# Optimization experiments

Measured on AMD Instinct MI355X. Metric: run time of the kernel, lower is better.

Reference implementation:

```python
import jax, jax.numpy as jnp
import numpy as np

HIDDEN = 1024
HEADS = 16
HEAD = HIDDEN // HEADS  # 64, rotary_emb_dim == head dim
B = 8
S = 1024  # max_seqlen; all sequences full length
WINDOW = (64, 64)  # sliding_window=128 -> (64, 64)
ROPE_BASE = 10000.0


def _rope_cos_sin(seqlen, dim, base):
    inv_freq = 1.0 / (base ** (jnp.arange(0, dim, 2, dtype=jnp.float32) / dim))
    t = jnp.arange(seqlen, dtype=jnp.float32)
    freqs = jnp.outer(t, inv_freq)  # [S, dim/2]
    return jnp.cos(freqs), jnp.sin(freqs)


def _apply_rope(x, cos, sin):
    # x: [B, S, H, D], non-interleaved rotary over full head dim
    d2 = cos.shape[-1]
    x1, x2 = x[..., :d2], x[..., d2:]
    c = cos[None, :, None, :]
    s = sin[None, :, None, :]
    return jnp.concatenate([x1 * c - x2 * s, x2 * c + x1 * s], axis=-1)


def setup_inputs() -> dict:
    key = jax.random.key(0)
    k1, k2, k3 = jax.random.split(key, 3)
    hidden_states = jax.random.normal(k1, (B * S, HIDDEN), dtype=jnp.float32)
    cu_seqlens = jnp.arange(B + 1, dtype=jnp.int32) * S
    indices = jnp.arange(B * S, dtype=jnp.int32)
    attn_mask = jnp.ones((B, S), dtype=jnp.int32)
    Wqkv = jax.random.normal(k2, (3 * HIDDEN, HIDDEN), dtype=jnp.float32) * 0.02
    Wo = jax.random.normal(k3, (HIDDEN, HIDDEN), dtype=jnp.float32) * 0.02
    return {
        'hidden_states': hidden_states,
        'cu_seqlens': cu_seqlens,
        'max_seqlen': S,
        'indices': indices,
        'attn_mask': attn_mask,
        'Wqkv': Wqkv,
        'Wo': Wo,
    }


def reference(hidden_states, cu_seqlens, max_seqlen, indices, attn_mask, Wqkv, Wo):
    # QKV projection on unpadded tokens: [T, 3*H*D]
    qkv = hidden_states @ Wqkv.T
    qkv = qkv.reshape(B, S, 3, HEADS, HEAD)
    # Rotary positions reset per sequence; all sequences are full length S.
    cos, sin = _rope_cos_sin(S, HEAD, ROPE_BASE)
    q = _apply_rope(qkv[:, :, 0], cos, sin)
    k = _apply_rope(qkv[:, :, 1], cos, sin)
    v = qkv[:, :, 2]
    scores = jnp.einsum('bshd,bthd->bhst', q, k) / jnp.sqrt(jnp.float32(HEAD))
    # sliding-window mask: key j visible to query i iff i-left <= j <= i+right
    i = jnp.arange(S)[:, None]
    j = jnp.arange(S)[None, :]
    win = (j >= i - WINDOW[0]) & (j <= i + WINDOW[1])  # [S, S]
    key_mask = attn_mask.astype(bool)[:, None, None, :]  # [B,1,1,S]
    mask = win[None, None, :, :] & key_mask
    scores = jnp.where(mask, scores, jnp.finfo(scores.dtype).min)
    probs = jax.nn.softmax(scores, axis=-1)
    attn = jnp.einsum('bhst,bthd->bshd', probs, v).reshape(B * S, HIDDEN)
    return attn @ Wo.T
```

## Files before the change

### kernel.cpp

```cpp
#include <hip/hip_runtime.h>


typedef __attribute__((ext_vector_type(8))) short short8;
typedef __attribute__((ext_vector_type(4))) float f32x4;

#define SEQ   1024
#define NHEAD 16
#define HEADD 64
#define NTOK  8192

__device__ __forceinline__ unsigned short f2bf(float x) {
  unsigned u = __float_as_uint(x);
  u += 0x7fffu + ((u >> 16) & 1u);
  return (unsigned short)(u >> 16);
}

__device__ __forceinline__ void gload_lds16(const void* g, void* l) {
  __builtin_amdgcn_global_load_lds((__attribute__((address_space(1))) void*)(g),
                                   (__attribute__((address_space(3))) void*)(l),
                                   16, 0, 0);
}

__global__ __launch_bounds__(256) void prep(
    const float* __restrict__ hidden, const float* __restrict__ Wqkv,
    const float* __restrict__ Wo,
    unsigned short* __restrict__ hb, unsigned short* __restrict__ wqb,
    unsigned short* __restrict__ wob, float2* __restrict__ tab) {
  int bid = blockIdx.x;
  const float* in; unsigned short* out; int i;
  if (bid < 8192)       { in = hidden; out = hb;  i = bid * 256 + threadIdx.x; }
  else if (bid < 11264) { in = Wqkv;   out = wqb; i = (bid - 8192) * 256 + threadIdx.x; }
  else if (bid < 12288) { in = Wo;     out = wob; i = (bid - 11264) * 256 + threadIdx.x; }
  else {
    int j = (bid - 12288) * 256 + threadIdx.x;
    int s = j >> 5, d = j & 31;
    float inv = exp2f(-(float)d * 0.41524101186092034f);
    float sn, cs;
    sincosf((float)s * inv, &sn, &cs);
    tab[j] = make_float2(cs, sn);
    return;
  }
  float4 v = ((const float4*)in)[i];
  ushort4 o;
  o.x = f2bf(v.x); o.y = f2bf(v.y); o.z = f2bf(v.z); o.w = f2bf(v.w);
  ((ushort4*)out)[i] = o;
}

__global__ __launch_bounds__(256) void gemm_qkv_rope(
    const unsigned short* __restrict__ A,
    const unsigned short* __restrict__ W,
    const float2* __restrict__ tab,
    unsigned short* __restrict__ qb,
    unsigned short* __restrict__ kb,
    unsigned short* __restrict__ vt)
{
  __shared__ unsigned short As[128 * 32];
  __shared__ unsigned short Bs[128 * 32];
  const int tid  = threadIdx.x;
  const int wave = tid >> 6, lane = tid & 63;
  const int quad = lane >> 4, l15 = lane & 15;
  const int bid  = blockIdx.x;
  const int xcd  = bid & 7, idx = bid >> 3;
  const int rb   = xcd * 8 + (idx & 7);
  const int cb   = idx >> 3;
  const int row0 = rb * 128;
  const int col0 = cb * 128;
  const int mrow = (wave >> 1) * 64;
  const int ncol = (wave & 1) * 64;
  const int qs8  = (quad ^ ((l15 >> 1) & 3)) * 8;

  f32x4 acc[4][4];
#pragma unroll
  for (int i = 0; i < 4; i++)
#pragma unroll
    for (int j = 0; j < 4; j++) acc[i][j] = (f32x4){0.f, 0.f, 0.f, 0.f};

  for (int k0 = 0; k0 < 1024; k0 += 32) {
#pragma unroll
    for (int i = 0; i < 2; i++) {
      int p = i * 256 + tid;
      int r = p >> 2, c = p & 3;
      int cs = c ^ ((r >> 1) & 3);
      gload_lds16(A + (size_t)(row0 + r) * 1024 + k0 + cs * 8, &As[p * 8]);
      gload_lds16(W + (size_t)(col0 + r) * 1024 + k0 + cs * 8, &Bs[p * 8]);
    }
    __syncthreads();
    short8 af[4], bf[4];
#pragma unroll
    for (int mt = 0; mt < 4; mt++)
      af[mt] = *(const short8*)&As[(mrow + mt * 16 + l15) * 32 + qs8];
#pragma unroll
    for (int nt = 0; nt < 4; nt++)
      bf[nt] = *(const short8*)&Bs[(ncol + nt * 16 + l15) * 32 + qs8];
#pragma unroll
    for (int mt = 0; mt < 4; mt++)
#pragma unroll
      for (int nt = 0; nt < 4; nt++)
        acc[mt][nt] = __builtin_amdgcn_mfma_f32_16x16x32_bf16(af[mt], bf[nt],
                                                              acc[mt][nt], 0, 0, 0);
    __syncthreads();
  }

  const int colw  = col0 + ncol;
  const int which = colw >> 10;
  const int h     = (colw >> 6) & 15;
  const int rowg  = row0 + mrow;

  if (which == 2) {
#pragma unroll
    for (int mt = 0; mt < 4; mt++) {
      int rbase = rowg + mt * 16 + quad * 4;
      int b = rbase >> 10, s = rbase & 1023;
#pragma unroll
      for (int c = 0; c < 4; c++) {
        int d = c * 16 + l15;
        ushort4 o;
        o.x = f2bf(acc[mt][c][0]); o.y = f2bf(acc[mt][c][1]);
        o.z = f2bf(acc[mt][c][2]); o.w = f2bf(acc[mt][c][3]);
        *(ushort4*)&vt[((size_t)((b * 16 + h) * 64 + d)) * 1024 + s] = o;
      }
    }
  } else {
    unsigned short* dst = (which == 0) ? qb : kb;
    const float scale = (which == 0) ? 0.125f : 1.0f;
#pragma unroll
    for (int mt = 0; mt < 4; mt++) {
#pragma unroll
      for (int r = 0; r < 4; r++) {
        int row = rowg + mt * 16 + quad * 4 + r;
        int b = row >> 10, s = row & 1023;
        size_t base = (size_t)((b * 16 + h) * 1024 + s) * 64;
        float2 t0 = tab[s * 32 + l15];
        float2 t1 = tab[s * 32 + 16 + l15];
        float x1a = acc[mt][0][r], x2a = acc[mt][2][r];
        float x1b = acc[mt][1][r], x2b = acc[mt][3][r];
        dst[base + l15]           = f2bf((x1a * t0.x - x2a * t0.y) * scale);
        dst[base + 32 + l15]      = f2bf((x2a * t0.x + x1a * t0.y) * scale);
        dst[base + 16 + l15]      = f2bf((x1b * t1.x - x2b * t1.y) * scale);
        dst[base + 48 + l15]      = f2bf((x2b * t1.x + x1b * t1.y) * scale);
      }
    }
  }
}

__global__ __launch_bounds__(256) void attn_win(
    const unsigned short* __restrict__ qb,
    const unsigned short* __restrict__ kb,
    const unsigned short* __restrict__ vt,
    const int* __restrict__ am,
    unsigned short* __restrict__ ob)
{
  __shared__ unsigned short Ks[192 * 68];
  __shared__ unsigned short Vs[64 * 196];
  __shared__ unsigned short smask[192];

  const int tid  = threadIdx.x;
  const int wave = tid >> 6, lane = tid & 63;
  const int quad = lane >> 4, l15 = lane & 15;
  const int b  = blockIdx.x >> 4, h = blockIdx.x & 15;
  const int qs = blockIdx.y * 64;
  const size_t hb = (size_t)(b * 16 + h);
  const unsigned short* Qg = qb + hb * SEQ * 64;
  const unsigned short* Kg = kb + hb * SEQ * 64;
  const unsigned short* Vg = vt + hb * 64 * SEQ;
  const int t0 = qs - 64;

#pragma unroll
  for (int i = 0; i < 6; i++) {
    int p = i * 256 + tid;
    int r = p >> 3, c = p & 7;
    int t = t0 + r; t = t < 0 ? 0 : (t > 1023 ? 1023 : t);
    *(short8*)&Ks[r * 68 + c * 8] = *(const short8*)&Kg[(size_t)t * 64 + c * 8];
  }
#pragma unroll
  for (int i = 0; i < 6; i++) {
    int p = i * 256 + tid;
    int d = p / 24, c = p % 24;
    int t = t0 + c * 8; t = t < 0 ? 0 : (t > 1016 ? 1016 : t);
    *(short8*)&Vs[d * 196 + c * 8] = *(const short8*)&Vg[(size_t)d * SEQ + t];
  }
  if (tid < 192) {
    int t = t0 + tid;
    smask[tid] = (t >= 0 && t < SEQ) ? (unsigned short)(am[b * SEQ + t] != 0) : 0;
  }
  __syncthreads();

  const int qw = qs + wave * 16;
  short8 qf0 = *(const short8*)&Qg[(size_t)(qw + l15) * 64 + quad * 8];
  short8 qf1 = *(const short8*)&Qg[(size_t)(qw + l15) * 64 + 32 + quad * 8];

  f32x4 sc[12];
#pragma unroll
  for (int tt = 0; tt < 12; tt++) {
    short8 b0 = *(const short8*)&Ks[(tt * 16 + l15) * 68 + quad * 8];
    short8 b1 = *(const short8*)&Ks[(tt * 16 + l15) * 68 + 32 + quad * 8];
    f32x4 a = (f32x4){0.f, 0.f, 0.f, 0.f};
    a = __builtin_amdgcn_mfma_f32_16x16x32_bf16(qf0, b0, a, 0, 0, 0);
    a = __builtin_amdgcn_mfma_f32_16x16x32_bf16(qf1, b1, a, 0, 0, 0);
    sc[tt] = a;
  }

  float lrow[4];
#pragma unroll
  for (int r = 0; r < 4; r++) {
    int i = qw + quad * 4 + r;
    float sum = 0.f;
#pragma unroll
    for (int tt = 0; tt < 12; tt++) {
      int t = t0 + tt * 16 + l15;
      bool ok = (t >= i - 64) && (t <= i + 64) && smask[tt * 16 + l15];
      float p = ok ? __expf(sc[tt][r]) : 0.f;
      sc[tt][r] = p;
      sum += p;
    }
#pragma unroll
    for (int off = 1; off < 16; off <<= 1) sum += __shfl_xor(sum, off);
    lrow[r] = sum;
  }

  __syncthreads();
  unsigned short* Pw = &Ks[wave * (16 * 196)];
#pragma unroll
  for (int tt = 0; tt < 12; tt++)
#pragma unroll
    for (int r = 0; r < 4; r++)
      Pw[(quad * 4 + r) * 196 + tt * 16 + l15] = f2bf(sc[tt][r]);
  __syncthreads();

  f32x4 o[4];
#pragma unroll
  for (int dt = 0; dt < 4; dt++) o[dt] = (f32x4){0.f, 0.f, 0.f, 0.f};
#pragma unroll
  for (int kt = 0; kt < 6; kt++) {
    short8 pf = *(const short8*)&Pw[l15 * 196 + kt * 32 + quad * 8];
#pragma unroll
    for (int dt = 0; dt < 4; dt++) {
      short8 vf = *(const short8*)&Vs[(dt * 16 + l15) * 196 + kt * 32 + quad * 8];
      o[dt] = __builtin_amdgcn_mfma_f32_16x16x32_bf16(pf, vf, o[dt], 0, 0, 0);
    }
  }

#pragma unroll
  for (int r = 0; r < 4; r++) {
    float inv = 1.f / lrow[r];
    int tok = b * SEQ + qw + quad * 4 + r;
    size_t base = (size_t)tok * 1024 + h * 64;
#pragma unroll
    for (int dt = 0; dt < 4; dt++)
      ob[base + dt * 16 + l15] = f2bf(o[dt][r] * inv);
  }
}

__global__ __launch_bounds__(256) void gemm_out(
    const unsigned short* __restrict__ A,
    const unsigned short* __restrict__ W,
    float* __restrict__ out)
{
  __shared__ unsigned short As[128 * 32];
  __shared__ unsigned short Bs[64 * 32];
  const int tid  = threadIdx.x;
  const int wave = tid >> 6, lane = tid & 63;
  const int quad = lane >> 4, l15 = lane & 15;
  const int bid  = blockIdx.x;
  const int xcd  = bid & 7, idx = bid >> 3;
  const int row0 = (xcd * 8 + (idx & 7)) * 128;
  const int col0 = (idx >> 3) * 64;
  const int mrow = (wave >> 1) * 64;
  const int ncol = (wave & 1) * 32;
  const int qs8  = (quad ^ ((l15 >> 1) & 3)) * 8;

  f32x4 acc[4][2];
#pragma unroll
  for (int i = 0; i < 4; i++)
#pragma unroll
    for (int j = 0; j < 2; j++) acc[i][j] = (f32x4){0.f, 0.f, 0.f, 0.f};

  for (int k0 = 0; k0 < 1024; k0 += 32) {
#pragma unroll
    for (int i = 0; i < 2; i++) {
      int p = i * 256 + tid;
      int r = p >> 2, c = p & 3;
      int cs = c ^ ((r >> 1) & 3);
      gload_lds16(A + (size_t)(row0 + r) * 1024 + k0 + cs * 8, &As[p * 8]);
    }
    {
      int p = tid;
      int r = p >> 2, c = p & 3;
      int cs = c ^ ((r >> 1) & 3);
      gload_lds16(W + (size_t)(col0 + r) * 1024 + k0 + cs * 8, &Bs[p * 8]);
    }
    __syncthreads();
    short8 af[4], bf[2];
#pragma unroll
    for (int mt = 0; mt < 4; mt++)
      af[mt] = *(const short8*)&As[(mrow + mt * 16 + l15) * 32 + qs8];
#pragma unroll
    for (int nt = 0; nt < 2; nt++)
      bf[nt] = *(const short8*)&Bs[(ncol + nt * 16 + l15) * 32 + qs8];
#pragma unroll
    for (int mt = 0; mt < 4; mt++)
#pragma unroll
      for (int nt = 0; nt < 2; nt++)
        acc[mt][nt] = __builtin_amdgcn_mfma_f32_16x16x32_bf16(af[mt], bf[nt],
                                                              acc[mt][nt], 0, 0, 0);
    __syncthreads();
  }

  const int colw = col0 + ncol;
  const int rowg = row0 + mrow;
#pragma unroll
  for (int mt = 0; mt < 4; mt++)
#pragma unroll
    for (int r = 0; r < 4; r++) {
      int row = rowg + mt * 16 + quad * 4 + r;
#pragma unroll
      for (int nt = 0; nt < 2; nt++)
        out[(size_t)row * 1024 + colw + nt * 16 + l15] = acc[mt][nt][r];
    }
}

extern "C" void kernel_launch(void* const* d_in, const int* in_sizes, int n_in,
                              void* d_out, int out_size, void* d_ws, size_t ws_size,
                              hipStream_t stream) {
  const float* hidden = (const float*)d_in[0];
  const int*   am     = (const int*)d_in[4];
  const float* Wqkv   = (const float*)d_in[5];
  const float* Wo     = (const float*)d_in[6];
  float* out = (float*)d_out;

  char* ws = (char*)d_ws;
  unsigned short* hb  = (unsigned short*)(ws);
  unsigned short* wqb = (unsigned short*)(ws + (size_t)(16 << 20));
  unsigned short* wob = (unsigned short*)(ws + (size_t)(22 << 20));
  unsigned short* qbf = (unsigned short*)(ws + (size_t)(24 << 20));
  unsigned short* kbf = (unsigned short*)(ws + (size_t)(40 << 20));
  unsigned short* vtb = (unsigned short*)(ws + (size_t)(56 << 20));
  float2*         tab = (float2*)(ws + (size_t)(72 << 20));
  unsigned short* ab  = hb;

  prep<<<12416, 256, 0, stream>>>(hidden, Wqkv, Wo, hb, wqb, wob, tab);

  gemm_qkv_rope<<<1536, 256, 0, stream>>>(hb, wqb, tab, qbf, kbf, vtb);

  dim3 g2(128, 16);
  attn_win<<<g2, 256, 0, stream>>>(qbf, kbf, vtb, am, ab);

  gemm_out<<<1024, 256, 0, stream>>>(ab, wob, out);
}
```

Before: 230.4 us.

## Double-buffer LDS and widen K tile to 64 in both projection GEMMs

Both the QKV-RoPE GEMM and the output GEMM now stage 64-wide K tiles into two LDS buffers. The next tile's global-to-LDS load is issued before computing on the current one, and the loop runs with one barrier per iteration instead of two. The swizzle changes to an 8-way XOR over 16-byte chunks to match the wider rows. The aim is to overlap global loads with MFMA work and halve loop and barrier overhead. In exchange LDS use per block grows fourfold (64 KB for the QKV kernel), which may cut occupancy.

After: 221.8 us. 3.8% less time.

```diff
diff --git a/kernel.cpp b/kernel.cpp
--- a/kernel.cpp
+++ b/kernel.cpp
@@ -54,8 +54,8 @@
     unsigned short* __restrict__ kb,
     unsigned short* __restrict__ vt)
 {
-  __shared__ unsigned short As[128 * 32];
-  __shared__ unsigned short Bs[128 * 32];
+  __shared__ unsigned short As[2][128 * 64];
+  __shared__ unsigned short Bs[2][128 * 64];
   const int tid  = threadIdx.x;
   const int wave = tid >> 6, lane = tid & 63;
   const int quad = lane >> 4, l15 = lane & 15;
@@ -67,7 +67,7 @@
   const int col0 = cb * 128;
   const int mrow = (wave >> 1) * 64;
   const int ncol = (wave & 1) * 64;
-  const int qs8  = (quad ^ ((l15 >> 1) & 3)) * 8;
+  const int l7x8 = (l15 & 7) * 8;
 
   f32x4 acc[4][4];
 #pragma unroll
@@ -75,30 +75,41 @@
 #pragma unroll
     for (int j = 0; j < 4; j++) acc[i][j] = (f32x4){0.f, 0.f, 0.f, 0.f};
 
-  for (int k0 = 0; k0 < 1024; k0 += 32) {
-#pragma unroll
-    for (int i = 0; i < 2; i++) {
+  auto stage = [&](int bi, int k0) {
+#pragma unroll
+    for (int i = 0; i < 4; i++) {
       int p = i * 256 + tid;
-      int r = p >> 2, c = p & 3;
-      int cs = c ^ ((r >> 1) & 3);
-      gload_lds16(A + (size_t)(row0 + r) * 1024 + k0 + cs * 8, &As[p * 8]);
-      gload_lds16(W + (size_t)(col0 + r) * 1024 + k0 + cs * 8, &Bs[p * 8]);
+      int r = p >> 3, c = p & 7;
+      int cs = c ^ (r & 7);
+      gload_lds16(A + (size_t)(row0 + r) * 1024 + k0 + cs * 8, &As[bi][p * 8]);
+      gload_lds16(W + (size_t)(col0 + r) * 1024 + k0 + cs * 8, &Bs[bi][p * 8]);
+    }
+  };
+
+  stage(0, 0);
+  __syncthreads();
+  int buf = 0;
+  for (int k0 = 0; k0 < 1024; k0 += 64) {
+    if (k0 + 64 < 1024) stage(buf ^ 1, k0 + 64);
+#pragma unroll
+    for (int kk = 0; kk < 2; kk++) {
+      const int qs8 = ((kk * 4 + quad) * 8) ^ l7x8;
+      short8 af[4], bfr[4];
+#pragma unroll
+      for (int mt = 0; mt < 4; mt++)
+        af[mt] = *(const short8*)&As[buf][(mrow + mt * 16 + l15) * 64 + qs8];
+#pragma unroll
+      for (int nt = 0; nt < 4; nt++)
+        bfr[nt] = *(const short8*)&Bs[buf][(ncol + nt * 16 + l15) * 64 + qs8];
+#pragma unroll
+      for (int mt = 0; mt < 4; mt++)
+#pragma unroll
+        for (int nt = 0; nt < 4; nt++)
+          acc[mt][nt] = __builtin_amdgcn_mfma_f32_16x16x32_bf16(af[mt], bfr[nt],
+                                                                acc[mt][nt], 0, 0, 0);
     }
     __syncthreads();
-    short8 af[4], bf[4];
-#pragma unroll
-    for (int mt = 0; mt < 4; mt++)
-      af[mt] = *(const short8*)&As[(mrow + mt * 16 + l15) * 32 + qs8];
-#pragma unroll
-    for (int nt = 0; nt < 4; nt++)
-      bf[nt] = *(const short8*)&Bs[(ncol + nt * 16 + l15) * 32 + qs8];
-#pragma unroll
-    for (int mt = 0; mt < 4; mt++)
-#pragma unroll
-      for (int nt = 0; nt < 4; nt++)
-        acc[mt][nt] = __builtin_amdgcn_mfma_f32_16x16x32_bf16(af[mt], bf[nt],
-                                                              acc[mt][nt], 0, 0, 0);
-    __syncthreads();
+    buf ^= 1;
   }
 
   const int colw  = col0 + ncol;
@@ -256,8 +267,8 @@
     const unsigned short* __restrict__ W,
     float* __restrict__ out)
 {
-  __shared__ unsigned short As[128 * 32];
-  __shared__ unsigned short Bs[64 * 32];
+  __shared__ unsigned short As[2][128 * 64];
+  __shared__ unsigned short Bs[2][64 * 64];
   const int tid  = threadIdx.x;
   const int wave = tid >> 6, lane = tid & 63;
   const int quad = lane >> 4, l15 = lane & 15;
@@ -267,7 +278,7 @@
   const int col0 = (idx >> 3) * 64;
   const int mrow = (wave >> 1) * 64;
   const int ncol = (wave & 1) * 32;
-  const int qs8  = (quad ^ ((l15 >> 1) & 3)) * 8;
+  const int l7x8 = (l15 & 7) * 8;
 
   f32x4 acc[4][2];
 #pragma unroll
@@ -275,35 +286,47 @@
 #pragma unroll
     for (int j = 0; j < 2; j++) acc[i][j] = (f32x4){0.f, 0.f, 0.f, 0.f};
 
-  for (int k0 = 0; k0 < 1024; k0 += 32) {
+  auto stage = [&](int bi, int k0) {
+#pragma unroll
+    for (int i = 0; i < 4; i++) {
+      int p = i * 256 + tid;
+      int r = p >> 3, c = p & 7;
+      int cs = c ^ (r & 7);
+      gload_lds16(A + (size_t)(row0 + r) * 1024 + k0 + cs * 8, &As[bi][p * 8]);
+    }
 #pragma unroll
     for (int i = 0; i < 2; i++) {
       int p = i * 256 + tid;
-      int r = p >> 2, c = p & 3;
-      int cs = c ^ ((r >> 1) & 3);
-      gload_lds16(A + (size_t)(row0 + r) * 1024 + k0 + cs * 8, &As[p * 8]);
-    }
-    {
-      int p = tid;
-      int r = p >> 2, c = p & 3;
-      int cs = c ^ ((r >> 1) & 3);
-      gload_lds16(W + (size_t)(col0 + r) * 1024 + k0 + cs * 8, &Bs[p * 8]);
+      int r = p >> 3, c = p & 7;
+      int cs = c ^ (r & 7);
+      gload_lds16(W + (size_t)(col0 + r) * 1024 + k0 + cs * 8, &Bs[bi][p * 8]);
+    }
+  };
+
+  stage(0, 0);
+  __syncthreads();
+  int buf = 0;
+  for (int k0 = 0; k0 < 1024; k0 += 64) {
+    if (k0 + 64 < 1024) stage(buf ^ 1, k0 + 64);
+#pragma unroll
+    for (int kk = 0; kk < 2; kk++) {
+      const int qs8 = ((kk * 4 + quad) * 8) ^ l7x8;
+      short8 af[4], bfr[2];
+#pragma unroll
+      for (int mt = 0; mt < 4; mt++)
+        af[mt] = *(const short8*)&As[buf][(mrow + mt * 16 + l15) * 64 + qs8];
+#pragma unroll
+      for (int nt = 0; nt < 2; nt++)
+        bfr[nt] = *(const short8*)&Bs[buf][(ncol + nt * 16 + l15) * 64 + qs8];
+#pragma unroll
+      for (int mt = 0; mt < 4; mt++)
+#pragma unroll
+        for (int nt = 0; nt < 2; nt++)
+          acc[mt][nt] = __builtin_amdgcn_mfma_f32_16x16x32_bf16(af[mt], bfr[nt],
+                                                                acc[mt][nt], 0, 0, 0);
     }
     __syncthreads();
-    short8 af[4], bf[2];
-#pragma unroll
-    for (int mt = 0; mt < 4; mt++)
-      af[mt] = *(const short8*)&As[(mrow + mt * 16 + l15) * 32 + qs8];
-#pragma unroll
-    for (int nt = 0; nt < 2; nt++)
-      bf[nt] = *(const short8*)&Bs[(ncol + nt * 16 + l15) * 32 + qs8];
-#pragma unroll
-    for (int mt = 0; mt < 4; mt++)
-#pragma unroll
-      for (int nt = 0; nt < 2; nt++)
-        acc[mt][nt] = __builtin_amdgcn_mfma_f32_16x16x32_bf16(af[mt], bf[nt],
-                                                              acc[mt][nt], 0, 0, 0);
-    __syncthreads();
+    buf ^= 1;
   }
 
   const int colw = col0 + ncol;
```
